# Optimization experiments

Hardware: AMD Instinct MI355X
Metric: run time of the kernel (lower is better)

The kernel has to match this reference:

```python
import jax, jax.numpy as jnp
import numpy as np

D_MODEL = 1024

def setup_inputs() -> dict:
    key = jax.random.key(0)
    ks = jax.random.split(key, 7)
    B, S, D = 4, 2048, D_MODEL
    scale = 1.0 / np.sqrt(D)
    x = jax.random.normal(ks[0], (B, S, D), dtype=jnp.float32)
    Wq = jax.random.normal(ks[1], (D, D), dtype=jnp.float32) * scale
    bq = jax.random.normal(ks[2], (D,), dtype=jnp.float32) * 0.02
    Wk = jax.random.normal(ks[3], (D, D), dtype=jnp.float32) * scale
    bk = jax.random.normal(ks[4], (D,), dtype=jnp.float32) * 0.02
    Wv = jax.random.normal(ks[5], (D, D), dtype=jnp.float32) * scale
    bv = jax.random.normal(ks[6], (D,), dtype=jnp.float32) * 0.02
    return {"x": x, "Wq": Wq, "bq": bq, "Wk": Wk, "bk": bk, "Wv": Wv, "bv": bv}

def reference(x, Wq, bq, Wk, bk, Wv, bv):
    # x: [B, S, D]
    B, S, D = x.shape
    q = jnp.einsum('bsd,de->bse', x, Wq) + bq
    k = jnp.einsum('bsd,de,->bse'.replace(',->', '->'), x, Wk) + bk
    v = jnp.einsum('bsd,de->bse', x, Wv) + bv
    # scores: [B, S, S], scaled by 1/sqrt(d_model) with additive causal mask
    scores = jnp.einsum('bqd,bkd->bqk', q, k) / jnp.sqrt(jnp.float32(D))
    causal = jnp.triu(jnp.full((S, S), -jnp.inf, dtype=scores.dtype), k=1)
    probs = jax.nn.softmax(scores + causal, axis=-1)
    return jnp.einsum('bqk,bkd->bqd', probs, v)
```

## Files before the change

### kernel.cpp

```cpp
#include <hip/hip_runtime.h>
#include <hip/hip_bf16.h>

#define S_LEN 2048
#define DM 1024
#define NB 4

typedef __attribute__((ext_vector_type(8))) short short8;
typedef __attribute__((ext_vector_type(4))) short short4v;
typedef __attribute__((ext_vector_type(4))) float floatx4;

__device__ inline short f2bf(float f) {
    union { float f; unsigned u; } v; v.f = f;
    unsigned r = 0x7fffu + ((v.u >> 16) & 1u);
    return (short)((v.u + r) >> 16);
}

__device__ inline void load16(const short* g, short* l) {
    __builtin_amdgcn_global_load_lds(
        (const __attribute__((address_space(1))) void*)g,
        (__attribute__((address_space(3))) void*)l,
        16, 0, 0);
}

__device__ inline void gemm_core64(const short* __restrict__ A,
                                   const short* __restrict__ Bt,
                                   int lda, int ldb, int kLen,
                                   int m0, int n0, floatx4 acc[4][4],
                                   short* As, short* Bs) {
    const int tid  = threadIdx.x;
    const int lane = tid & 63;
    const int wave = tid >> 6;
    const int wr   = (wave >> 1) * 64;
    const int wc   = (wave & 1) * 64;
    const int quad = lane >> 4;
    const int l16  = lane & 15;

    const short* gA[4]; const short* gB[4];
    short* lA[4]; short* lB[4];
#pragma unroll
    for (int c = 0; c < 4; c++) {
        int idx = c * 256 + tid;
        int row = idx >> 3;
        int g = (idx & 7) ^ (row & 7);
        gA[c] = A  + (size_t)(m0 + row) * lda + g * 8;
        gB[c] = Bt + (size_t)(n0 + row) * ldb + g * 8;
        int lbase = (c * 256 + wave * 64) * 8;
        lA[c] = &As[lbase];
        lB[c] = &Bs[lbase];
    }

    const short* fa[2]; const short* fb[2];
#pragma unroll
    for (int h = 0; h < 2; h++) {
        int sw = ((h * 4 + quad) ^ (l16 & 7)) * 8;
        fa[h] = &As[(wr + l16) * 64 + sw];
        fb[h] = &Bs[(wc + l16) * 64 + sw];
    }

    for (int k0 = 0; k0 < kLen; k0 += 64) {
#pragma unroll
        for (int c = 0; c < 4; c++) load16(gA[c], lA[c]);
#pragma unroll
        for (int c = 0; c < 4; c++) load16(gB[c], lB[c]);
#pragma unroll
        for (int c = 0; c < 4; c++) { gA[c] += 64; gB[c] += 64; }
        __syncthreads();

#pragma unroll
        for (int h = 0; h < 2; h++) {
            short8 af[4], bf[4];
#pragma unroll
            for (int t = 0; t < 4; t++) af[t] = *(const short8*)(fa[h] + t * 1024);
#pragma unroll
            for (int t = 0; t < 4; t++) bf[t] = *(const short8*)(fb[h] + t * 1024);
#pragma unroll
            for (int mt = 0; mt < 4; mt++)
#pragma unroll
                for (int nt = 0; nt < 4; nt++)
                    acc[mt][nt] = __builtin_amdgcn_mfma_f32_16x16x32_bf16(
                        af[mt], bf[nt], acc[mt][nt], 0, 0, 0);
        }
        __syncthreads();
    }
}

__global__ void prep(const float* __restrict__ x,
                     const float* __restrict__ Wq, const float* __restrict__ Wk,
                     const float* __restrict__ Wv,
                     short* __restrict__ xb, short* __restrict__ Wt,
                     float* __restrict__ denom) {
    __shared__ float t[64][65];
    int bid = blockIdx.x, tid = threadIdx.x;
    if (bid < 768) {
        int w = bid >> 8, tl = bid & 255;
        const float* W = (w == 0) ? Wq : (w == 1) ? Wk : Wv;
        short* out = Wt + (size_t)w * DM * DM;
        int bx = (tl & 15) * 64;
        int by = (tl >> 4) * 64;
        int tx = tid & 63, ty = tid >> 6;
        for (int r = ty; r < 64; r += 4)
            t[r][tx] = W[(size_t)(by + r) * DM + bx + tx];
        __syncthreads();
        for (int r = ty; r < 64; r += 4)
            out[(size_t)(bx + r) * DM + by + tx] = f2bf(t[tx][r]);
    } else if (bid < 768 + 8192) {
        int i = (bid - 768) * 256 + tid;
        float4 v = ((const float4*)x)[i];
        short4v o;
        o.x = f2bf(v.x); o.y = f2bf(v.y); o.z = f2bf(v.z); o.w = f2bf(v.w);
        ((short4v*)xb)[i] = o;
    } else {
        int i = (bid - 8960) * 256 + tid;
        if (i < NB * S_LEN) denom[i] = 0.f;
    }
}

__global__ __launch_bounds__(256, 2)
void qkv_fused(const short* __restrict__ xb, const short* __restrict__ Wt,
               const float* __restrict__ bq, const float* __restrict__ bk,
               const float* __restrict__ bv,
               short* __restrict__ Qb, short* __restrict__ Kb,
               short* __restrict__ Vtb) {
    __shared__ short As[8192];
    __shared__ short Bs[3 * 8192];
    int n0 = blockIdx.x * 128;
    int m0 = blockIdx.y * 128;

    const int tid  = threadIdx.x;
    const int lane = tid & 63;
    const int wave = tid >> 6;
    const int wr   = (wave >> 1) * 64;
    const int wc   = (wave & 1) * 64;
    const int quad = lane >> 4;
    const int l16  = lane & 15;

    floatx4 acc[3][4][4];
#pragma unroll
    for (int w = 0; w < 3; w++)
#pragma unroll
        for (int i = 0; i < 4; i++)
#pragma unroll
            for (int j = 0; j < 4; j++) acc[w][i][j] = (floatx4){0.f, 0.f, 0.f, 0.f};

    const short* gA[4]; const short* gW[4];
    short* lA[4]; short* lB[4];
#pragma unroll
    for (int c = 0; c < 4; c++) {
        int idx = c * 256 + tid;
        int row = idx >> 3;
        int g = (idx & 7) ^ (row & 7);
        gA[c] = xb + (size_t)(m0 + row) * DM + g * 8;
        gW[c] = Wt + (size_t)(n0 + row) * DM + g * 8;
        int lbase = (c * 256 + wave * 64) * 8;
        lA[c] = &As[lbase];
        lB[c] = &Bs[lbase];
    }

    const short* fa[2]; const short* fb[2];
#pragma unroll
    for (int h = 0; h < 2; h++) {
        int sw = ((h * 4 + quad) ^ (l16 & 7)) * 8;
        fa[h] = &As[(wr + l16) * 64 + sw];
        fb[h] = &Bs[(wc + l16) * 64 + sw];
    }

    for (int k0 = 0; k0 < DM; k0 += 64) {
#pragma unroll
        for (int c = 0; c < 4; c++) load16(gA[c], lA[c]);
#pragma unroll
        for (int w = 0; w < 3; w++)
#pragma unroll
            for (int c = 0; c < 4; c++)
                load16(gW[c] + (size_t)w * DM * DM, lB[c] + w * 8192);
#pragma unroll
        for (int c = 0; c < 4; c++) { gA[c] += 64; gW[c] += 64; }
        __syncthreads();

#pragma unroll
        for (int h = 0; h < 2; h++) {
            short8 af[4];
#pragma unroll
            for (int t = 0; t < 4; t++) af[t] = *(const short8*)(fa[h] + t * 1024);
#pragma unroll
            for (int w = 0; w < 3; w++) {
                short8 bf[4];
#pragma unroll
                for (int t = 0; t < 4; t++)
                    bf[t] = *(const short8*)(fb[h] + w * 8192 + t * 1024);
#pragma unroll
                for (int mt = 0; mt < 4; mt++)
#pragma unroll
                    for (int nt = 0; nt < 4; nt++)
                        acc[w][mt][nt] = __builtin_amdgcn_mfma_f32_16x16x32_bf16(
                            af[mt], bf[nt], acc[w][mt][nt], 0, 0, 0);
            }
        }
        __syncthreads();
    }

#pragma unroll
    for (int w = 0; w < 2; w++) {
        short* out = w ? Kb : Qb;
        const float* bias = w ? bk : bq;
        float scale = w ? 1.0f : 0.03125f;
#pragma unroll
        for (int mt = 0; mt < 4; mt++)
#pragma unroll
            for (int nt = 0; nt < 4; nt++) {
                int col = n0 + wc + nt * 16 + l16;
                float bv_ = bias[col];
#pragma unroll
                for (int r = 0; r < 4; r++) {
                    int row = m0 + wr + mt * 16 + quad * 4 + r;
                    out[(size_t)row * DM + col] = f2bf((acc[w][mt][nt][r] + bv_) * scale);
                }
            }
    }

    {
        int b = m0 >> 11;
        int sbase = (m0 & 2047) + wr;
        float bvv[4];
#pragma unroll
        for (int nt = 0; nt < 4; nt++) bvv[nt] = bv[n0 + wc + nt * 16 + l16];
        short* buf = (wave & 1) ? Bs : As;
        short* vt = Vtb + ((size_t)b * DM + n0 + wc) * S_LEN;
#pragma unroll
        for (int p = 0; p < 2; p++) {
            __syncthreads();
            if ((wave >> 1) == p) {
#pragma unroll
                for (int mt = 0; mt < 4; mt++)
#pragma unroll
                    for (int nt = 0; nt < 4; nt++) {
                        int c = nt * 16 + l16;
                        short4v pk;
                        pk.x = f2bf(acc[2][mt][nt][0] + bvv[nt]);
                        pk.y = f2bf(acc[2][mt][nt][1] + bvv[nt]);
                        pk.z = f2bf(acc[2][mt][nt][2] + bvv[nt]);
                        pk.w = f2bf(acc[2][mt][nt][3] + bvv[nt]);
                        *(short4v*)&buf[c * 72 + mt * 16 + quad * 4] = pk;
                    }
                asm volatile("s_waitcnt lgkmcnt(0)" ::: "memory");
#pragma unroll
                for (int ps = 0; ps < 8; ps++) {
                    int dl = ps * 8 + (lane >> 3);
                    int sl = (lane & 7) * 8;
                    short8 row = *(short8*)&buf[dl * 72 + sl];
                    *(short8*)(vt + (size_t)dl * S_LEN + sbase + sl) = row;
                }
            }
        }
    }
}

__global__ __launch_bounds__(256, 3)
void score_gemm(const short* __restrict__ Qb, const short* __restrict__ Kb,
                short* __restrict__ P, float* __restrict__ denom) {
    __shared__ short As[8192];
    __shared__ short Bs[8192];
    int b = blockIdx.z;
    int xq = blockIdx.x;
    int it = (int)((sqrtf(8.0f * xq + 1.0f) - 1.0f) * 0.5f);
    while ((it + 1) * (it + 2) / 2 <= xq) it++;
    while (it * (it + 1) / 2 > xq) it--;
    int jt = xq - it * (it + 1) / 2;
    int n0 = jt * 128, m0 = it * 128;
    const short* A  = Qb + (size_t)b * S_LEN * DM;
    const short* Bt = Kb + (size_t)b * S_LEN * DM;

    floatx4 acc[4][4];
#pragma unroll
    for (int i = 0; i < 4; i++)
#pragma unroll
        for (int j = 0; j < 4; j++) acc[i][j] = (floatx4){0.f, 0.f, 0.f, 0.f};

    gemm_core64(A, Bt, DM, DM, DM, m0, n0, acc, As, Bs);

    short* out = P + (size_t)b * S_LEN * S_LEN;
    float* dsum = denom + (size_t)b * S_LEN;
    const int lane = threadIdx.x & 63, wave = threadIdx.x >> 6;
    const int wr = (wave >> 1) * 64, wc = (wave & 1) * 64;
    const int quad = lane >> 4, l16 = lane & 15;
    const bool diag = (jt == it);
#pragma unroll
    for (int mt = 0; mt < 4; mt++) {
#pragma unroll
        for (int r = 0; r < 4; r++) {
            int row = m0 + wr + mt * 16 + quad * 4 + r;
            float psum = 0.f;
#pragma unroll
            for (int nt = 0; nt < 4; nt++) {
                int col = n0 + wc + nt * 16 + l16;
                float e = __expf(acc[mt][nt][r]);
                if (diag && col > row) e = 0.f;
                out[(size_t)row * S_LEN + col] = f2bf(e);
                psum += e;
            }
#pragma unroll
            for (int off = 8; off > 0; off >>= 1)
                psum += __shfl_down(psum, off, 16);
            if (l16 == 0) atomicAdd(&dsum[row], psum);
        }
    }
}

__global__ __launch_bounds__(256, 3)
void pv_gemm(const short* __restrict__ P, const short* __restrict__ Vtb,
             const float* __restrict__ denom, float* __restrict__ O) {
    __shared__ short As[8192];
    __shared__ short Bs[8192];
    int b = blockIdx.z;
    int n0 = blockIdx.x * 128;
    int it = (int)(gridDim.y - 1 - blockIdx.y);
    int m0 = it * 128;
    int kLen = (it + 1) * 128;
    const short* A  = P   + (size_t)b * S_LEN * S_LEN;
    const short* Bt = Vtb + (size_t)b * DM * S_LEN;

    floatx4 acc[4][4];
#pragma unroll
    for (int i = 0; i < 4; i++)
#pragma unroll
        for (int j = 0; j < 4; j++) acc[i][j] = (floatx4){0.f, 0.f, 0.f, 0.f};

    gemm_core64(A, Bt, S_LEN, S_LEN, kLen, m0, n0, acc, As, Bs);

    float* out = O + (size_t)b * S_LEN * DM;
    const float* dsum = denom + (size_t)b * S_LEN;
    const int lane = threadIdx.x & 63, wave = threadIdx.x >> 6;
    const int wr = (wave >> 1) * 64, wc = (wave & 1) * 64;
    const int quad = lane >> 4, l16 = lane & 15;
#pragma unroll
    for (int mt = 0; mt < 4; mt++) {
#pragma unroll
        for (int r = 0; r < 4; r++) {
            int row = m0 + wr + mt * 16 + quad * 4 + r;
            float inv = 1.0f / dsum[row];
#pragma unroll
            for (int nt = 0; nt < 4; nt++) {
                int col = n0 + wc + nt * 16 + l16;
                out[(size_t)row * DM + col] = acc[mt][nt][r] * inv;
            }
        }
    }
}

extern "C" void kernel_launch(void* const* d_in, const int* in_sizes, int n_in,
                              void* d_out, int out_size, void* d_ws, size_t ws_size,
                              hipStream_t stream) {
    const float* x  = (const float*)d_in[0];
    const float* Wq = (const float*)d_in[1];
    const float* bq = (const float*)d_in[2];
    const float* Wk = (const float*)d_in[3];
    const float* bk = (const float*)d_in[4];
    const float* Wv = (const float*)d_in[5];
    const float* bv = (const float*)d_in[6];
    float* out = (float*)d_out;

    char* ws = (char*)d_ws;
    const size_t MB = 1u << 20;
    short* xb    = (short*)(ws + 0);
    short* Wt    = (short*)(ws + 16 * MB);
    short* Qb    = (short*)(ws + 22 * MB);
    short* Kb    = (short*)(ws + 38 * MB);
    short* Vtb   = (short*)(ws + 54 * MB);
    short* P     = (short*)(ws + 70 * MB);
    float* denom = (float*)(ws + 102 * MB);

    prep<<<dim3(8992), dim3(256), 0, stream>>>(x, Wq, Wk, Wv, xb, Wt, denom);
    qkv_fused<<<dim3(8, 64), dim3(256), 0, stream>>>(xb, Wt, bq, bk, bv, Qb, Kb, Vtb);
    score_gemm<<<dim3(136, 1, NB), dim3(256), 0, stream>>>(Qb, Kb, P, denom);
    pv_gemm<<<dim3(8, 16, NB), dim3(256), 0, stream>>>(P, Vtb, denom, out);
}
```

Before: 222.5 us.

## Widen score and PV GEMM tiles to 128x256 with paired causal tiles

The shared gemm_core64 helper is inlined into score_gemm and pv_gemm, and each block's output tile grows from 128x128 to 128x256. Each wave now holds a 64x128 accumulator, and the B tile in LDS doubles in size. The score kernel enumerates pairs of column tiles along the causal triangle and applies the causal mask on every tile, which computes some tiles above the diagonal that are then zeroed. The goal is more MFMA work per LDS load and less operand refetch. In exchange the blocks per launch are halved, launch bounds drop to 2 blocks per CU, register pressure rises, and load balance on 256 CUs may suffer.

Result: slower. 230.2 us (+3.5%).

```diff
diff --git a/kernel.cpp b/kernel.cpp
--- a/kernel.cpp
+++ b/kernel.cpp
@@ -20,68 +20,6 @@
         (const __attribute__((address_space(1))) void*)g,
         (__attribute__((address_space(3))) void*)l,
         16, 0, 0);
-}
-
-__device__ inline void gemm_core64(const short* __restrict__ A,
-                                   const short* __restrict__ Bt,
-                                   int lda, int ldb, int kLen,
-                                   int m0, int n0, floatx4 acc[4][4],
-                                   short* As, short* Bs) {
-    const int tid  = threadIdx.x;
-    const int lane = tid & 63;
-    const int wave = tid >> 6;
-    const int wr   = (wave >> 1) * 64;
-    const int wc   = (wave & 1) * 64;
-    const int quad = lane >> 4;
-    const int l16  = lane & 15;
-
-    const short* gA[4]; const short* gB[4];
-    short* lA[4]; short* lB[4];
-#pragma unroll
-    for (int c = 0; c < 4; c++) {
-        int idx = c * 256 + tid;
-        int row = idx >> 3;
-        int g = (idx & 7) ^ (row & 7);
-        gA[c] = A  + (size_t)(m0 + row) * lda + g * 8;
-        gB[c] = Bt + (size_t)(n0 + row) * ldb + g * 8;
-        int lbase = (c * 256 + wave * 64) * 8;
-        lA[c] = &As[lbase];
-        lB[c] = &Bs[lbase];
-    }
-
-    const short* fa[2]; const short* fb[2];
-#pragma unroll
-    for (int h = 0; h < 2; h++) {
-        int sw = ((h * 4 + quad) ^ (l16 & 7)) * 8;
-        fa[h] = &As[(wr + l16) * 64 + sw];
-        fb[h] = &Bs[(wc + l16) * 64 + sw];
-    }
-
-    for (int k0 = 0; k0 < kLen; k0 += 64) {
-#pragma unroll
-        for (int c = 0; c < 4; c++) load16(gA[c], lA[c]);
-#pragma unroll
-        for (int c = 0; c < 4; c++) load16(gB[c], lB[c]);
-#pragma unroll
-        for (int c = 0; c < 4; c++) { gA[c] += 64; gB[c] += 64; }
-        __syncthreads();
-
-#pragma unroll
-        for (int h = 0; h < 2; h++) {
-            short8 af[4], bf[4];
-#pragma unroll
-            for (int t = 0; t < 4; t++) af[t] = *(const short8*)(fa[h] + t * 1024);
-#pragma unroll
-            for (int t = 0; t < 4; t++) bf[t] = *(const short8*)(fb[h] + t * 1024);
-#pragma unroll
-            for (int mt = 0; mt < 4; mt++)
-#pragma unroll
-                for (int nt = 0; nt < 4; nt++)
-                    acc[mt][nt] = __builtin_amdgcn_mfma_f32_16x16x32_bf16(
-                        af[mt], bf[nt], acc[mt][nt], 0, 0, 0);
-        }
-        __syncthreads();
-    }
 }
 
 __global__ void prep(const float* __restrict__ x,
@@ -254,35 +192,76 @@
     }
 }
 
-__global__ __launch_bounds__(256, 3)
+__global__ __launch_bounds__(256, 2)
 void score_gemm(const short* __restrict__ Qb, const short* __restrict__ Kb,
                 short* __restrict__ P, float* __restrict__ denom) {
     __shared__ short As[8192];
-    __shared__ short Bs[8192];
+    __shared__ short Bs[16384];
     int b = blockIdx.z;
     int xq = blockIdx.x;
-    int it = (int)((sqrtf(8.0f * xq + 1.0f) - 1.0f) * 0.5f);
-    while ((it + 1) * (it + 2) / 2 <= xq) it++;
-    while (it * (it + 1) / 2 > xq) it--;
-    int jt = xq - it * (it + 1) / 2;
-    int n0 = jt * 128, m0 = it * 128;
+    int it = 0, base = 0;
+    while (xq >= base + ((it + 2) >> 1)) { base += (it + 2) >> 1; it++; }
+    int jt0 = (xq - base) * 2;
+    int m0 = it * 128, n0 = jt0 * 128;
     const short* A  = Qb + (size_t)b * S_LEN * DM;
     const short* Bt = Kb + (size_t)b * S_LEN * DM;
 
-    floatx4 acc[4][4];
+    const int tid  = threadIdx.x;
+    const int lane = tid & 63;
+    const int wave = tid >> 6;
+    const int wr   = (wave >> 1) * 64;
+    const int wc   = (wave & 1) * 128;
+    const int quad = lane >> 4;
+    const int l16  = lane & 15;
+
+    floatx4 acc[4][8];
 #pragma unroll
     for (int i = 0; i < 4; i++)
 #pragma unroll
-        for (int j = 0; j < 4; j++) acc[i][j] = (floatx4){0.f, 0.f, 0.f, 0.f};
-
-    gemm_core64(A, Bt, DM, DM, DM, m0, n0, acc, As, Bs);
+        for (int j = 0; j < 8; j++) acc[i][j] = (floatx4){0.f, 0.f, 0.f, 0.f};
+
+    int rowc = tid >> 3;
+    int g = (tid & 7) ^ (rowc & 7);
+    const short* gA0 = A  + (size_t)(m0 + rowc) * DM + g * 8;
+    const short* gB0 = Bt + (size_t)(n0 + rowc) * DM + g * 8;
+    short* lA0 = &As[wave * 512];
+    short* lB0 = &Bs[wave * 512];
+
+    const short* fa[2]; const short* fb[2];
+#pragma unroll
+    for (int h = 0; h < 2; h++) {
+        int sw = ((h * 4 + quad) ^ (l16 & 7)) * 8;
+        fa[h] = &As[(wr + l16) * 64 + sw];
+        fb[h] = &Bs[(wc + l16) * 64 + sw];
+    }
+
+    for (int k0 = 0; k0 < DM; k0 += 64) {
+#pragma unroll
+        for (int c = 0; c < 4; c++) load16(gA0 + (size_t)c * 32 * DM, lA0 + c * 2048);
+#pragma unroll
+        for (int c = 0; c < 8; c++) load16(gB0 + (size_t)c * 32 * DM, lB0 + c * 2048);
+        gA0 += 64; gB0 += 64;
+        __syncthreads();
+
+#pragma unroll
+        for (int h = 0; h < 2; h++) {
+            short8 af[4], bf[8];
+#pragma unroll
+            for (int t = 0; t < 4; t++) af[t] = *(const short8*)(fa[h] + t * 1024);
+#pragma unroll
+            for (int t = 0; t < 8; t++) bf[t] = *(const short8*)(fb[h] + t * 1024);
+#pragma unroll
+            for (int mt = 0; mt < 4; mt++)
+#pragma unroll
+                for (int nt = 0; nt < 8; nt++)
+                    acc[mt][nt] = __builtin_amdgcn_mfma_f32_16x16x32_bf16(
+                        af[mt], bf[nt], acc[mt][nt], 0, 0, 0);
+        }
+        __syncthreads();
+    }
 
     short* out = P + (size_t)b * S_LEN * S_LEN;
     float* dsum = denom + (size_t)b * S_LEN;
-    const int lane = threadIdx.x & 63, wave = threadIdx.x >> 6;
-    const int wr = (wave >> 1) * 64, wc = (wave & 1) * 64;
-    const int quad = lane >> 4, l16 = lane & 15;
-    const bool diag = (jt == it);
 #pragma unroll
     for (int mt = 0; mt < 4; mt++) {
 #pragma unroll
@@ -290,10 +269,10 @@
             int row = m0 + wr + mt * 16 + quad * 4 + r;
             float psum = 0.f;
 #pragma unroll
-            for (int nt = 0; nt < 4; nt++) {
+            for (int nt = 0; nt < 8; nt++) {
                 int col = n0 + wc + nt * 16 + l16;
                 float e = __expf(acc[mt][nt][r]);
-                if (diag && col > row) e = 0.f;
+                if (col > row) e = 0.f;
                 out[(size_t)row * S_LEN + col] = f2bf(e);
                 psum += e;
             }
@@ -305,32 +284,75 @@
     }
 }
 
-__global__ __launch_bounds__(256, 3)
+__global__ __launch_bounds__(256, 2)
 void pv_gemm(const short* __restrict__ P, const short* __restrict__ Vtb,
              const float* __restrict__ denom, float* __restrict__ O) {
     __shared__ short As[8192];
-    __shared__ short Bs[8192];
+    __shared__ short Bs[16384];
     int b = blockIdx.z;
-    int n0 = blockIdx.x * 128;
+    int n0 = blockIdx.x * 256;
     int it = (int)(gridDim.y - 1 - blockIdx.y);
     int m0 = it * 128;
     int kLen = (it + 1) * 128;
     const short* A  = P   + (size_t)b * S_LEN * S_LEN;
     const short* Bt = Vtb + (size_t)b * DM * S_LEN;
 
-    floatx4 acc[4][4];
+    const int tid  = threadIdx.x;
+    const int lane = tid & 63;
+    const int wave = tid >> 6;
+    const int wr   = (wave >> 1) * 64;
+    const int wc   = (wave & 1) * 128;
+    const int quad = lane >> 4;
+    const int l16  = lane & 15;
+
+    floatx4 acc[4][8];
 #pragma unroll
     for (int i = 0; i < 4; i++)
 #pragma unroll
-        for (int j = 0; j < 4; j++) acc[i][j] = (floatx4){0.f, 0.f, 0.f, 0.f};
-
-    gemm_core64(A, Bt, S_LEN, S_LEN, kLen, m0, n0, acc, As, Bs);
+        for (int j = 0; j < 8; j++) acc[i][j] = (floatx4){0.f, 0.f, 0.f, 0.f};
+
+    int rowc = tid >> 3;
+    int g = (tid & 7) ^ (rowc & 7);
+    const short* gA0 = A  + (size_t)(m0 + rowc) * S_LEN + g * 8;
+    const short* gB0 = Bt + (size_t)(n0 + rowc) * S_LEN + g * 8;
+    short* lA0 = &As[wave * 512];
+    short* lB0 = &Bs[wave * 512];
+
+    const short* fa[2]; const short* fb[2];
+#pragma unroll
+    for (int h = 0; h < 2; h++) {
+        int sw = ((h * 4 + quad) ^ (l16 & 7)) * 8;
+        fa[h] = &As[(wr + l16) * 64 + sw];
+        fb[h] = &Bs[(wc + l16) * 64 + sw];
+    }
+
+    for (int k0 = 0; k0 < kLen; k0 += 64) {
+#pragma unroll
+        for (int c = 0; c < 4; c++) load16(gA0 + (size_t)c * 32 * S_LEN, lA0 + c * 2048);
+#pragma unroll
+        for (int c = 0; c < 8; c++) load16(gB0 + (size_t)c * 32 * S_LEN, lB0 + c * 2048);
+        gA0 += 64; gB0 += 64;
+        __syncthreads();
+
+#pragma unroll
+        for (int h = 0; h < 2; h++) {
+            short8 af[4], bf[8];
+#pragma unroll
+            for (int t = 0; t < 4; t++) af[t] = *(const short8*)(fa[h] + t * 1024);
+#pragma unroll
+            for (int t = 0; t < 8; t++) bf[t] = *(const short8*)(fb[h] + t * 1024);
+#pragma unroll
+            for (int mt = 0; mt < 4; mt++)
+#pragma unroll
+                for (int nt = 0; nt < 8; nt++)
+                    acc[mt][nt] = __builtin_amdgcn_mfma_f32_16x16x32_bf16(
+                        af[mt], bf[nt], acc[mt][nt], 0, 0, 0);
+        }
+        __syncthreads();
+    }
 
     float* out = O + (size_t)b * S_LEN * DM;
     const float* dsum = denom + (size_t)b * S_LEN;
-    const int lane = threadIdx.x & 63, wave = threadIdx.x >> 6;
-    const int wr = (wave >> 1) * 64, wc = (wave & 1) * 64;
-    const int quad = lane >> 4, l16 = lane & 15;
 #pragma unroll
     for (int mt = 0; mt < 4; mt++) {
 #pragma unroll
@@ -338,7 +360,7 @@
             int row = m0 + wr + mt * 16 + quad * 4 + r;
             float inv = 1.0f / dsum[row];
 #pragma unroll
-            for (int nt = 0; nt < 4; nt++) {
+            for (int nt = 0; nt < 8; nt++) {
                 int col = n0 + wc + nt * 16 + l16;
                 out[(size_t)row * DM + col] = acc[mt][nt][r] * inv;
             }
@@ -370,6 +392,6 @@
 
     prep<<<dim3(8992), dim3(256), 0, stream>>>(x, Wq, Wk, Wv, xb, Wt, denom);
     qkv_fused<<<dim3(8, 64), dim3(256), 0, stream>>>(xb, Wt, bq, bk, bv, Qb, Kb, Vtb);
-    score_gemm<<<dim3(136, 1, NB), dim3(256), 0, stream>>>(Qb, Kb, P, denom);
-    pv_gemm<<<dim3(8, 16, NB), dim3(256), 0, stream>>>(P, Vtb, denom, out);
-}
+    score_gemm<<<dim3(72, 1, NB), dim3(256), 0, stream>>>(Qb, Kb, P, denom);
+    pv_gemm<<<dim3(4, 16, NB), dim3(256), 0, stream>>>(P, Vtb, denom, out);
+}
```
